# Optimization experiments

Hardware: AMD Instinct MI355X
Metric: run time of the kernel (lower is better)

## Reference

```python
import jax, jax.numpy as jnp
import numpy as np

SCALING = 2.0  # lora scaling attached via set_lora (lora_alpha / r)


def setup_inputs() -> dict:
    key = jax.random.key(0)
    ks = jax.random.split(key, 8)
    E, DIN, DOUT, N, K, R = 8, 2048, 2048, 4096, 2, 16
    inputs = jax.random.normal(ks[0], (N, DIN), jnp.float32)
    weight = jax.random.normal(ks[1], (E, DOUT, DIN), jnp.float32) * 0.02
    lora_A = jax.random.normal(ks[2], (E, R, DIN), jnp.float32) * 0.02
    lora_B = jax.random.normal(ks[3], (E, DOUT, R), jnp.float32) * 0.02
    gates = jax.nn.softmax(jax.random.normal(ks[4], (N, K), jnp.float32), axis=-1)
    # expert assignment per (token, slot); scattermoe contract:
    #   sorted_scattered_idxs = argsort(assign); token = idx // k, slot = idx % k
    assign = jax.random.randint(ks[5], (N * K,), 0, E)
    sorted_scattered_idxs = jnp.argsort(assign).astype(jnp.int32)
    sorted_expert_idxs = assign[sorted_scattered_idxs].astype(jnp.int32)
    counts = jnp.bincount(assign, length=E)
    expert_offsets = jnp.cumsum(counts).astype(jnp.int32)
    return dict(inputs=inputs, weight=weight, lora_A=lora_A, lora_B=lora_B,
                gates=gates, sorted_expert_idxs=sorted_expert_idxs,
                sorted_scattered_idxs=sorted_scattered_idxs,
                expert_offsets=expert_offsets, k=K)


def reference(inputs, weight, lora_A, lora_B, gates, sorted_expert_idxs,
              sorted_scattered_idxs, expert_offsets, k):
    # Fused LoRA grouped GEMM:  Y = X @ W + scaling * (X @ A^T) @ B^T
    # grouped_in=False, grouped_out=False, bias=None (module defaults).
    E = weight.shape[0]
    N = gates.shape[0]
    W = jnp.swapaxes(weight, 1, 2)          # [E, din, dout] (weight.permute(0,2,1))
    token = sorted_scattered_idxs // k      # source token per sorted slot
    slot = sorted_scattered_idxs % k        # which of the k routes
    x = inputs[token]                       # gather -> [N*k, din]
    y = jnp.zeros((x.shape[0], W.shape[2]), x.dtype)
    for e in range(E):                      # fixed small expert loop
        m = (sorted_expert_idxs == e)[:, None]
        xe = jnp.where(m, x, 0.0)
        y = y + (xe @ W[e] + SCALING * ((xe @ jnp.swapaxes(lora_A[e], 0, 1)) @ jnp.swapaxes(lora_B[e], 0, 1)))
    g = gates[token, slot][:, None]         # gate per sorted slot
    out = jnp.zeros((N, W.shape[2]), y.dtype).at[token].add(y * g)
    return out
```

## Files before the change

### kernel.cpp

```cpp
#include <hip/hip_runtime.h>
#include <hip/hip_bf16.h>

#define E_    8
#define DIN   2048
#define DOUT  2048
#define N_TOK 4096
#define NK    8192
#define R_    16
#define KEXT  2112
#define KT_N  (KEXT / 64)
#define BM    256
#define BN    256
#define MT_MAX 40

typedef __bf16 bf16x8 __attribute__((ext_vector_type(8)));
typedef float  f32x4  __attribute__((ext_vector_type(4)));

static __device__ __forceinline__ void gld16(const void* g, void* l) {
  __builtin_amdgcn_global_load_lds(
      (const __attribute__((address_space(1))) unsigned int*)g,
      (__attribute__((address_space(3))) unsigned int*)l, 16, 0, 0);
}

static __device__ __forceinline__ unsigned short f2bfu(float f) {
  union { float f; unsigned int u; } v; v.f = f;
  unsigned int r = v.u + 0x7fffu + ((v.u >> 16) & 1u);
  return (unsigned short)(r >> 16);
}

__global__ void __launch_bounds__(64)
k_wconv(const float* __restrict__ w, const float* __restrict__ lb,
        unsigned short* __restrict__ wbe) {
  const long long row = blockIdx.x;
  const float4* src  = (const float4*)(w + row * DIN);
  const float4* lsrc = (const float4*)(lb + row * R_);
  ushort4* dst = (ushort4*)(wbe + row * KEXT);
  for (int u = threadIdx.x; u < KEXT / 4; u += 64) {
    float4 v;
    if (u < 512)       v = src[u];
    else if (u < 516)  v = lsrc[u - 512];
    else               v = make_float4(0.f, 0.f, 0.f, 0.f);
    ushort4 o;
    o.x = f2bfu(v.x); o.y = f2bfu(v.y); o.z = f2bfu(v.z); o.w = f2bfu(v.w);
    dst[u] = o;
  }
}

__global__ void k_gather(const float* __restrict__ x, const int* __restrict__ ssi,
                         const float* __restrict__ gates, const int* __restrict__ kptr,
                         unsigned short* __restrict__ Xe, float* __restrict__ gate,
                         int* __restrict__ tok,
                         const float* __restrict__ la, unsigned short* __restrict__ Ab) {
  int s = blockIdx.x;
  int ai = (s << 8) + threadIdx.x;
  if (ai < (E_ * R_ * DIN / 4)) {
    float4 v = ((const float4*)la)[ai];
    ushort4 o;
    o.x = f2bfu(v.x); o.y = f2bfu(v.y); o.z = f2bfu(v.z); o.w = f2bfu(v.w);
    ((ushort4*)Ab)[ai] = o;
  }
  int ssv = ssi[s];
  int kk = kptr[0];
  int t = ssv / kk, sl = ssv - t * kk;
  if (threadIdx.x == 0) { gate[s] = gates[t * kk + sl]; tok[s] = t; }
  const float4* src = (const float4*)(x + (long long)t * DIN);
  ushort4* dst = (ushort4*)(Xe + (long long)s * KEXT);
  for (int i = threadIdx.x; i < 512; i += 256) {
    float4 v = src[i];
    ushort4 o;
    o.x = f2bfu(v.x); o.y = f2bfu(v.y); o.z = f2bfu(v.z); o.w = f2bfu(v.w);
    dst[i] = o;
  }
  if (threadIdx.x < 12) {
    ushort4 z; z.x = z.y = z.z = z.w = 0;
    dst[516 + threadIdx.x] = z;
  }
}

__global__ void __launch_bounds__(64)
k_xa(unsigned short* __restrict__ Xe, const unsigned short* __restrict__ Ab,
     const int* __restrict__ eoff) {
  int tile = blockIdx.x;
  int off_prev = 0, e = -1, m_start = 0, m_end = 0, acc_t = 0;
#pragma unroll
  for (int i = 0; i < E_; i++) {
    int oe = eoff[i];
    int te = (oe - off_prev + 15) >> 4;
    if (e < 0 && tile < acc_t + te) {
      e = i; m_start = off_prev + (tile - acc_t) * 16; m_end = oe;
    }
    acc_t += te; off_prev = oe;
  }
  if (e < 0) return;
  const int lane = threadIdx.x;
  const int l15 = lane & 15, quad = lane >> 4;
  int arow = m_start + l15; if (arow >= m_end) arow = m_end - 1;
  const unsigned short* xp = Xe + (long long)arow * KEXT + quad * 8;
  const unsigned short* bp = Ab + ((long long)e * R_ + l15) * DIN + quad * 8;
  f32x4 acc = (f32x4){0.f, 0.f, 0.f, 0.f};
#pragma unroll 8
  for (int k0 = 0; k0 < DIN; k0 += 32) {
    bf16x8 a = *(const bf16x8*)(xp + k0);
    bf16x8 b = *(const bf16x8*)(bp + k0);
    acc = __builtin_amdgcn_mfma_f32_16x16x32_bf16(a, b, acc, 0, 0, 0);
  }
#pragma unroll
  for (int t = 0; t < 4; t++) {
    int slot = m_start + quad * 4 + t;
    if (slot < m_end)
      Xe[(long long)slot * KEXT + 2048 + l15] = f2bfu(2.0f * acc[t]);
  }
}

__global__ void __launch_bounds__(512, 2)
k_gemm(const unsigned short* __restrict__ Xe, const unsigned short* __restrict__ Wbe,
       const float* __restrict__ gate, const int* __restrict__ tok,
       const int* __restrict__ eoff, float* __restrict__ out) {
  __shared__ alignas(16) unsigned short sA[2][BM * 64];
  __shared__ alignas(16) unsigned short sB[2][BN * 64];
  __shared__ float gs[BM];
  __shared__ int   ts[BM];

  const int id  = blockIdx.x;
  const int xcd = id & 7;
  const int jb  = id >> 3;
  const int nt  = jb & 7;
  const int mt  = ((jb >> 3) << 3) | xcd;
  const int n_start = nt << 8;

  int off_prev = 0, e = -1, m_start = 0, m_end = 0, acc_t = 0;
#pragma unroll
  for (int i = 0; i < E_; i++) {
    int oe = eoff[i];
    int te = (oe - off_prev + 255) >> 8;
    if (e < 0 && mt < acc_t + te) {
      e = i; m_start = off_prev + (mt - acc_t) * 256; m_end = oe;
    }
    acc_t += te;
    off_prev = oe;
  }
  if (e < 0) return;

  const int tid = threadIdx.x;
  const int w = tid >> 6, lane = tid & 63;
  const int wm = w >> 2, wn = w & 3;
  const int quad = lane >> 4, l15 = lane & 15;
  const int srow = lane >> 3;
  const int scol = ((lane & 7) ^ srow) * 8;

  if (tid < 256) {
    int gm = m_start + tid; if (gm >= m_end) gm = m_end - 1;
    gs[tid] = gate[gm];
    ts[tid] = tok[gm];
  }

  f32x4 acc[8][4];
#pragma unroll
  for (int mi = 0; mi < 8; mi++)
#pragma unroll
    for (int ni = 0; ni < 4; ni++)
      acc[mi][ni] = (f32x4){0.f, 0.f, 0.f, 0.f};

  const unsigned short* Wb = Wbe + (long long)e * DOUT * KEXT;

#define STAGE(buf, kt_)                                                              \
  {                                                                                  \
    const int k0s = (kt_) * 64;                                                      \
    _Pragma("unroll")                                                                \
    for (int jj = 0; jj < 4; jj++) {                                                 \
      const int c = (w << 2) + jj;                                                   \
      const int rt = (c << 3) + srow;                                                \
      int ga = m_start + rt; if (ga >= m_end) ga = m_end - 1;     \
      gld16(Xe + (long long)ga * KEXT + k0s + scol, &sA[buf][(c << 9) + (lane << 3)]); \
      gld16(Wb + (long long)(n_start + rt) * KEXT + k0s + scol,                      \
            &sB[buf][(c << 9) + (lane << 3)]);                                       \
    }                                                                                \
  }

  STAGE(0, 0);
  __syncthreads();

  for (int kt = 0; kt < KT_N; kt++) {
    const int b = kt & 1;
    if (kt + 1 < KT_N) STAGE(b ^ 1, kt + 1);
#pragma unroll
    for (int ks = 0; ks < 2; ks++) {
      const int kx = (((ks << 2) | quad) ^ (l15 & 7)) << 3;
      bf16x8 af[8], bfr[4];
#pragma unroll
      for (int mi = 0; mi < 8; mi++)
        af[mi] = *(const bf16x8*)&sA[b][(wm * 128 + mi * 16 + l15) * 64 + kx];
#pragma unroll
      for (int ni = 0; ni < 4; ni++)
        bfr[ni] = *(const bf16x8*)&sB[b][(wn * 64 + ni * 16 + l15) * 64 + kx];
#pragma unroll
      for (int mi = 0; mi < 8; mi++)
#pragma unroll
        for (int ni = 0; ni < 4; ni++)
          acc[mi][ni] = __builtin_amdgcn_mfma_f32_16x16x32_bf16(
              af[mi], bfr[ni], acc[mi][ni], 0, 0, 0);
    }
    __syncthreads();
  }
#undef STAGE

#pragma unroll
  for (int mi = 0; mi < 8; mi++) {
    const int rbase = wm * 128 + mi * 16 + quad * 4;
#pragma unroll
    for (int t4 = 0; t4 < 4; t4++) {
      const int row = rbase + t4;
      if (m_start + row >= m_end) continue;
      const float g = gs[row];
      float* orow = out + (long long)ts[row] * DOUT + n_start + wn * 64 + l15;
#pragma unroll
      for (int ni = 0; ni < 4; ni++)
        atomicAdd(orow + ni * 16, acc[mi][ni][t4] * g);
    }
  }
}

extern "C" void kernel_launch(void* const* d_in, const int* in_sizes, int n_in,
                              void* d_out, int out_size, void* d_ws, size_t ws_size,
                              hipStream_t stream) {
  (void)in_sizes; (void)n_in; (void)out_size; (void)ws_size;
  const float* inputs = (const float*)d_in[0];
  const float* weight = (const float*)d_in[1];
  const float* lora_A = (const float*)d_in[2];
  const float* lora_B = (const float*)d_in[3];
  const float* gates  = (const float*)d_in[4];
  const int* sei  = (const int*)d_in[5];
  const int* ssi  = (const int*)d_in[6];
  const int* eoff = (const int*)d_in[7];
  const int* kptr = (const int*)d_in[8];
  (void)sei;
  float* out = (float*)d_out;

  unsigned char* ws = (unsigned char*)d_ws;
  unsigned short* Wbe = (unsigned short*)ws;
  unsigned short* Xe  = (unsigned short*)(ws + 69206016);
  unsigned short* Ab  = (unsigned short*)(ws + 103809024);
  float* gate = (float*)(ws + 104333312);
  int*   tok  = (int*)(ws + 104366080);

  hipMemsetAsync(d_out, 0, (size_t)N_TOK * DOUT * sizeof(float), stream);
  k_wconv<<<E_ * DOUT, 64, 0, stream>>>(weight, lora_B, Wbe);
  k_gather<<<NK, 256, 0, stream>>>(inputs, ssi, gates, kptr, Xe, gate, tok, lora_A, Ab);
  k_xa<<<519, 64, 0, stream>>>(Xe, Ab, eoff);
  k_gemm<<<MT_MAX * 8, 512, 0, stream>>>(Xe, Wbe, gate, tok, eoff, out);
}
```

Before: 442.7 us.

## Split GEMM along K, fuse prep kernels, parallelize XA over waves

Splits the main grouped GEMM into two K halves, doubling the block count to fill more CUs, with both halves atomically accumulating into the output. Merges weight conversion, token gather and lora_A conversion into one launch, and spreads the X·A^T reduction across four waves with an LDS reduction. Replaces __syncthreads with explicit vmcnt waits and raw barriers so the next tile's loads can stay in flight. The cost is double the atomic output traffic and a changed tile-to-XCD mapping.

```diff
diff --git a/kernel.cpp b/kernel.cpp
--- a/kernel.cpp
+++ b/kernel.cpp
@@ -28,58 +28,61 @@
   return (unsigned short)(r >> 16);
 }
 
-__global__ void __launch_bounds__(64)
-k_wconv(const float* __restrict__ w, const float* __restrict__ lb,
-        unsigned short* __restrict__ wbe) {
-  const long long row = blockIdx.x;
-  const float4* src  = (const float4*)(w + row * DIN);
-  const float4* lsrc = (const float4*)(lb + row * R_);
-  ushort4* dst = (ushort4*)(wbe + row * KEXT);
-  for (int u = threadIdx.x; u < KEXT / 4; u += 64) {
-    float4 v;
-    if (u < 512)       v = src[u];
-    else if (u < 516)  v = lsrc[u - 512];
-    else               v = make_float4(0.f, 0.f, 0.f, 0.f);
+__global__ void __launch_bounds__(256)
+k_prep(const float* __restrict__ w, const float* __restrict__ lb,
+       unsigned short* __restrict__ wbe,
+       const float* __restrict__ la, unsigned short* __restrict__ Ab,
+       const float* __restrict__ x, const int* __restrict__ ssi,
+       const float* __restrict__ gates, const int* __restrict__ kptr,
+       unsigned short* __restrict__ Xe, float* __restrict__ gate,
+       int* __restrict__ tok) {
+  const int b = blockIdx.x, tid = threadIdx.x;
+  if (b < 4096) {
+    const int wv = tid >> 6, ln = tid & 63;
+    const long long row = ((long long)b << 2) | wv;
+    const float4* src  = (const float4*)(w + row * DIN);
+    const float4* lsrc = (const float4*)(lb + row * R_);
+    ushort4* dst = (ushort4*)(wbe + row * KEXT);
+    for (int u = ln; u < KEXT / 4; u += 64) {
+      float4 v;
+      if (u < 512)       v = src[u];
+      else if (u < 516)  v = lsrc[u - 512];
+      else               v = make_float4(0.f, 0.f, 0.f, 0.f);
+      ushort4 o;
+      o.x = f2bfu(v.x); o.y = f2bfu(v.y); o.z = f2bfu(v.z); o.w = f2bfu(v.w);
+      dst[u] = o;
+    }
+  } else if (b < 12288) {
+    const int s = b - 4096;
+    int ssv = ssi[s];
+    int kk = kptr[0];
+    int t = ssv / kk, sl = ssv - t * kk;
+    if (tid == 0) { gate[s] = gates[t * kk + sl]; tok[s] = t; }
+    const float4* src = (const float4*)(x + (long long)t * DIN);
+    ushort4* dst = (ushort4*)(Xe + (long long)s * KEXT);
+    for (int i = tid; i < 512; i += 256) {
+      float4 v = src[i];
+      ushort4 o;
+      o.x = f2bfu(v.x); o.y = f2bfu(v.y); o.z = f2bfu(v.z); o.w = f2bfu(v.w);
+      dst[i] = o;
+    }
+    if (tid < 12) {
+      ushort4 z; z.x = z.y = z.z = z.w = 0;
+      dst[516 + tid] = z;
+    }
+  } else {
+    const int i = ((b - 12288) << 8) + tid;
+    float4 v = ((const float4*)la)[i];
     ushort4 o;
     o.x = f2bfu(v.x); o.y = f2bfu(v.y); o.z = f2bfu(v.z); o.w = f2bfu(v.w);
-    dst[u] = o;
-  }
-}
-
-__global__ void k_gather(const float* __restrict__ x, const int* __restrict__ ssi,
-                         const float* __restrict__ gates, const int* __restrict__ kptr,
-                         unsigned short* __restrict__ Xe, float* __restrict__ gate,
-                         int* __restrict__ tok,
-                         const float* __restrict__ la, unsigned short* __restrict__ Ab) {
-  int s = blockIdx.x;
-  int ai = (s << 8) + threadIdx.x;
-  if (ai < (E_ * R_ * DIN / 4)) {
-    float4 v = ((const float4*)la)[ai];
-    ushort4 o;
-    o.x = f2bfu(v.x); o.y = f2bfu(v.y); o.z = f2bfu(v.z); o.w = f2bfu(v.w);
-    ((ushort4*)Ab)[ai] = o;
-  }
-  int ssv = ssi[s];
-  int kk = kptr[0];
-  int t = ssv / kk, sl = ssv - t * kk;
-  if (threadIdx.x == 0) { gate[s] = gates[t * kk + sl]; tok[s] = t; }
-  const float4* src = (const float4*)(x + (long long)t * DIN);
-  ushort4* dst = (ushort4*)(Xe + (long long)s * KEXT);
-  for (int i = threadIdx.x; i < 512; i += 256) {
-    float4 v = src[i];
-    ushort4 o;
-    o.x = f2bfu(v.x); o.y = f2bfu(v.y); o.z = f2bfu(v.z); o.w = f2bfu(v.w);
-    dst[i] = o;
-  }
-  if (threadIdx.x < 12) {
-    ushort4 z; z.x = z.y = z.z = z.w = 0;
-    dst[516 + threadIdx.x] = z;
-  }
-}
-
-__global__ void __launch_bounds__(64)
+    ((ushort4*)Ab)[i] = o;
+  }
+}
+
+__global__ void __launch_bounds__(256)
 k_xa(unsigned short* __restrict__ Xe, const unsigned short* __restrict__ Ab,
      const int* __restrict__ eoff) {
+  __shared__ f32x4 red[4][64];
   int tile = blockIdx.x;
   int off_prev = 0, e = -1, m_start = 0, m_end = 0, acc_t = 0;
 #pragma unroll
@@ -92,23 +95,29 @@
     acc_t += te; off_prev = oe;
   }
   if (e < 0) return;
-  const int lane = threadIdx.x;
+  const int tid = threadIdx.x;
+  const int wv = tid >> 6, lane = tid & 63;
   const int l15 = lane & 15, quad = lane >> 4;
   int arow = m_start + l15; if (arow >= m_end) arow = m_end - 1;
-  const unsigned short* xp = Xe + (long long)arow * KEXT + quad * 8;
-  const unsigned short* bp = Ab + ((long long)e * R_ + l15) * DIN + quad * 8;
+  const unsigned short* xp = Xe + (long long)arow * KEXT + wv * 512 + quad * 8;
+  const unsigned short* bp = Ab + ((long long)e * R_ + l15) * DIN + wv * 512 + quad * 8;
   f32x4 acc = (f32x4){0.f, 0.f, 0.f, 0.f};
 #pragma unroll 8
-  for (int k0 = 0; k0 < DIN; k0 += 32) {
+  for (int k0 = 0; k0 < 512; k0 += 32) {
     bf16x8 a = *(const bf16x8*)(xp + k0);
     bf16x8 b = *(const bf16x8*)(bp + k0);
     acc = __builtin_amdgcn_mfma_f32_16x16x32_bf16(a, b, acc, 0, 0, 0);
   }
-#pragma unroll
-  for (int t = 0; t < 4; t++) {
-    int slot = m_start + quad * 4 + t;
-    if (slot < m_end)
-      Xe[(long long)slot * KEXT + 2048 + l15] = f2bfu(2.0f * acc[t]);
+  red[wv][lane] = acc;
+  __syncthreads();
+  if (wv == 0) {
+    f32x4 s = red[0][lane] + red[1][lane] + red[2][lane] + red[3][lane];
+#pragma unroll
+    for (int t = 0; t < 4; t++) {
+      int slot = m_start + quad * 4 + t;
+      if (slot < m_end)
+        Xe[(long long)slot * KEXT + 2048 + l15] = f2bfu(2.0f * s[t]);
+    }
   }
 }
 
@@ -122,10 +131,10 @@
   __shared__ int   ts[BM];
 
   const int id  = blockIdx.x;
-  const int xcd = id & 7;
+  const int nt  = id & 7;
   const int jb  = id >> 3;
-  const int nt  = jb & 7;
-  const int mt  = ((jb >> 3) << 3) | xcd;
+  const int kh  = jb & 1;
+  const int mt  = jb >> 1;
   const int n_start = nt << 8;
 
   int off_prev = 0, e = -1, m_start = 0, m_end = 0, acc_t = 0;
@@ -177,12 +186,22 @@
     }                                                                                \
   }
 
-  STAGE(0, 0);
-  __syncthreads();
-
-  for (int kt = 0; kt < KT_N; kt++) {
-    const int b = kt & 1;
-    if (kt + 1 < KT_N) STAGE(b ^ 1, kt + 1);
+  const int kt_beg = kh * 17;
+  const int kt_end = kh ? KT_N : 17;
+
+  asm volatile("s_waitcnt vmcnt(0) lgkmcnt(0)" ::: "memory");
+  STAGE(0, kt_beg);
+
+  for (int kt = kt_beg; kt < kt_end; ++kt) {
+    const int b = (kt - kt_beg) & 1;
+    if (kt + 1 < kt_end) {
+      STAGE(b ^ 1, kt + 1);
+      asm volatile("s_waitcnt vmcnt(8)" ::: "memory");
+    } else {
+      asm volatile("s_waitcnt vmcnt(0)" ::: "memory");
+    }
+    __builtin_amdgcn_s_barrier();
+    __builtin_amdgcn_sched_barrier(0);
 #pragma unroll
     for (int ks = 0; ks < 2; ks++) {
       const int kx = (((ks << 2) | quad) ^ (l15 & 7)) << 3;
@@ -200,7 +219,9 @@
           acc[mi][ni] = __builtin_amdgcn_mfma_f32_16x16x32_bf16(
               af[mi], bfr[ni], acc[mi][ni], 0, 0, 0);
     }
-    __syncthreads();
+    asm volatile("" ::: "memory");
+    __builtin_amdgcn_s_barrier();
+    __builtin_amdgcn_sched_barrier(0);
   }
 #undef STAGE
 
@@ -244,8 +265,8 @@
   int*   tok  = (int*)(ws + 104366080);
 
   hipMemsetAsync(d_out, 0, (size_t)N_TOK * DOUT * sizeof(float), stream);
-  k_wconv<<<E_ * DOUT, 64, 0, stream>>>(weight, lora_B, Wbe);
-  k_gather<<<NK, 256, 0, stream>>>(inputs, ssi, gates, kptr, Xe, gate, tok, lora_A, Ab);
-  k_xa<<<519, 64, 0, stream>>>(Xe, Ab, eoff);
-  k_gemm<<<MT_MAX * 8, 512, 0, stream>>>(Xe, Wbe, gate, tok, eoff, out);
-}
+  k_prep<<<4096 + 8192 + 256, 256, 0, stream>>>(weight, lora_B, Wbe, lora_A, Ab,
+                                                inputs, ssi, gates, kptr, Xe, gate, tok);
+  k_xa<<<519, 256, 0, stream>>>(Xe, Ab, eoff);
+  k_gemm<<<MT_MAX * 8 * 2, 512, 0, stream>>>(Xe, Wbe, gate, tok, eoff, out);
+}
```

After: 446.9 us. No clear change (+0.9%).
